# Optimization experiments

Measured on AMD Instinct MI355X. Metric: run time of the kernel, lower is better.

## Reference

```python
import jax, jax.numpy as jnp
import numpy as np

H, I, E, S, K = 768, 3072, 16, 2, 2
SCALE = 1.0  # routed_scaling_factor


def setup_inputs() -> dict:
    key = jax.random.key(0)
    ks = jax.random.split(key, 8)
    sd = 0.02
    return {
        "hidden_states": jax.random.normal(ks[0], (2, 1024, H), jnp.float32),
        "gate_w": jax.random.normal(ks[1], (E, H), jnp.float32) * sd,   # router nn.Linear(H,E).weight
        "shared_wg": jax.random.normal(ks[2], (S, H, I), jnp.float32) * sd,
        "shared_wu": jax.random.normal(ks[3], (S, H, I), jnp.float32) * sd,
        "shared_wd": jax.random.normal(ks[4], (S, I, H), jnp.float32) * sd,
        "wg": jax.random.normal(ks[5], (E, H, I), jnp.float32) * sd,
        "wu": jax.random.normal(ks[6], (E, H, I), jnp.float32) * sd,
        "wd": jax.random.normal(ks[7], (E, I, H), jnp.float32) * sd,
    }


def reference(hidden_states, gate_w, shared_wg, shared_wu, shared_wd, wg, wu, wd):
    B, T, _ = hidden_states.shape
    x = hidden_states.reshape(-1, H)                       # [N, H], N = B*T
    N = x.shape[0]

    # ---- shared experts: always-on, averaged ----
    g = jnp.einsum('nh,shi->sni', x, shared_wg)
    u = jnp.einsum('nh,shi->sni', x, shared_wu)
    shared_out = jnp.einsum('sni,sih->snh', jax.nn.silu(g) * u, shared_wd).mean(axis=0)

    # ---- router: softmax scores, top-k, renormalize, scale ----
    router_logits = x @ gate_w.T                           # [N, E]
    routing_weights = jax.nn.softmax(router_logits, axis=-1)
    topk_w, topk_idx = jax.lax.top_k(routing_weights, K)   # [N, K]
    topk_w = topk_w / (topk_w.sum(axis=-1, keepdims=True) + 1e-8)
    topk_w = topk_w * SCALE

    # combine weights: [N, E], zero for non-selected experts (duplicates summed,
    # matching the torch per-token weight-sum semantics)
    combine = jnp.zeros((N, E), x.dtype).at[jnp.arange(N)[:, None], topk_idx].add(topk_w)

    # ---- routed experts: weighted combine (w=0 for unselected -> same math) ----
    ge = jnp.einsum('nh,ehi->eni', x, wg)                  # [E, N, I]
    ue = jnp.einsum('nh,ehi->eni', x, wu)
    ye = jnp.einsum('eni,eih->enh', jax.nn.silu(ge) * ue, wd)  # [E, N, H]
    routed_out = jnp.einsum('ne,enh->nh', combine, ye)

    return (shared_out + routed_out).reshape(B, T, H)
```

## Files before the change

### kernel.cpp

```cpp
#include <hip/hip_runtime.h>
#include <hip/hip_bf16.h>

#define H 768
#define I_DIM 3072
#define NEXP 16
#define TOPK 2

typedef __bf16 bf16;
typedef __bf16 bf16x4 __attribute__((ext_vector_type(4)));
typedef __bf16 bf16x8 __attribute__((ext_vector_type(8)));
typedef float f32x4 __attribute__((ext_vector_type(4)));

__device__ __forceinline__ int swizzle_mtile(int bx, int gx) {
    int per = gx >> 3;
    if ((per << 3) != gx) return bx;
    return (bx & 7) * per + (bx >> 3);
}

__global__ void cvt_x_kernel(const float* __restrict__ x, bf16* __restrict__ xb, int n) {
    int i = (blockIdx.x * blockDim.x + threadIdx.x) * 8;
    if (i >= n) return;
    f32x4 v0 = *(const f32x4*)(x + i);
    f32x4 v1 = *(const f32x4*)(x + i + 4);
    bf16x8 p;
#pragma unroll
    for (int j = 0; j < 4; j++) { p[j] = (bf16)v0[j]; p[4 + j] = (bf16)v1[j]; }
    *(bf16x8*)(xb + i) = p;
}

__global__ __launch_bounds__(256) void transpose_cvt_kernel(
        const float* __restrict__ in, bf16* __restrict__ outp, int R, int C) {
    __shared__ bf16 t[64][74];
    const float* ip = in + (size_t)blockIdx.z * R * C;
    bf16* op = outp + (size_t)blockIdx.z * R * C;
    int c0 = blockIdx.x * 64, r0 = blockIdx.y * 64;
    int tid = threadIdx.x;
    int lr = tid >> 4, lc = (tid & 15) * 4;
#pragma unroll
    for (int p = 0; p < 4; p++) {
        int r = p * 16 + lr;
        f32x4 v = *(const f32x4*)(ip + (size_t)(r0 + r) * C + (c0 + lc));
        bf16x4 b;
#pragma unroll
        for (int j = 0; j < 4; j++) b[j] = (bf16)v[j];
        *(bf16x4*)&t[r][lc] = b;
    }
    __syncthreads();
    int oc = tid >> 2, s = (tid & 3) * 16;
    bf16x8 o0, o1;
#pragma unroll
    for (int j = 0; j < 8; j++) { o0[j] = t[s + j][oc]; o1[j] = t[s + 8 + j][oc]; }
    *(bf16x8*)(op + (size_t)(c0 + oc) * R + (r0 + s)) = o0;
    *(bf16x8*)(op + (size_t)(c0 + oc) * R + (r0 + s + 8)) = o1;
}

__global__ void router_kernel(const float* __restrict__ x, const float* __restrict__ gw,
                              int* __restrict__ tk_e, float* __restrict__ tk_w,
                              int* __restrict__ counts, int N) {
    int wave = threadIdx.x >> 6;
    int lane = threadIdx.x & 63;
    int t = blockIdx.x * 4 + wave;
    if (t >= N) return;
    const float* xr = x + (size_t)t * H;
    float acc[NEXP];
#pragma unroll
    for (int e = 0; e < NEXP; e++) acc[e] = 0.f;
    for (int h0 = 0; h0 < H; h0 += 64) {
        float xv = xr[h0 + lane];
#pragma unroll
        for (int e = 0; e < NEXP; e++) acc[e] += xv * gw[e * H + h0 + lane];
    }
#pragma unroll
    for (int e = 0; e < NEXP; e++) {
#pragma unroll
        for (int off = 32; off > 0; off >>= 1) acc[e] += __shfl_xor(acc[e], off);
    }
    if (lane == 0) {
        float m = acc[0];
#pragma unroll
        for (int e = 1; e < NEXP; e++) m = fmaxf(m, acc[e]);
        float p[NEXP]; float z = 0.f;
#pragma unroll
        for (int e = 0; e < NEXP; e++) { p[e] = expf(acc[e] - m); z += p[e]; }
        float inv = 1.f / z;
#pragma unroll
        for (int e = 0; e < NEXP; e++) p[e] *= inv;
        int i0 = 0; float v0 = p[0];
#pragma unroll
        for (int e = 1; e < NEXP; e++) if (p[e] > v0) { v0 = p[e]; i0 = e; }
        int i1 = -1; float v1 = -1.f;
#pragma unroll
        for (int e = 0; e < NEXP; e++) if (e != i0 && p[e] > v1) { v1 = p[e]; i1 = e; }
        float s = 1.f / (v0 + v1 + 1e-8f);
        tk_e[t * 2 + 0] = i0; tk_w[t * 2 + 0] = v0 * s;
        tk_e[t * 2 + 1] = i1; tk_w[t * 2 + 1] = v1 * s;
        atomicAdd(&counts[i0], 1);
        atomicAdd(&counts[i1], 1);
    }
}

__global__ void scan_fill_kernel(const int* __restrict__ counts, int* __restrict__ cursors,
                                 int* __restrict__ pad_off, int* __restrict__ rows_token,
                                 float* __restrict__ rows_weight, int N) {
    __shared__ int s_total;
    if (threadIdx.x == 0) {
        int off = 0;
        for (int e = 0; e < NEXP; e++) {
            pad_off[e] = off;
            cursors[e] = off;
            off += (counts[e] + 127) & ~127;
        }
        pad_off[NEXP] = off;
        s_total = off;
    }
    __syncthreads();
    int total = s_total;
    for (int r = threadIdx.x; r < 2 * N; r += blockDim.x) {
        rows_token[r] = r & (N - 1);
        rows_weight[r] = 0.5f;
    }
    for (int r = threadIdx.x; r < total; r += blockDim.x) {
        rows_token[2 * N + r] = 0;
        rows_weight[2 * N + r] = 0.f;
    }
}

__global__ void scatter_kernel(const int* __restrict__ tk_e, const float* __restrict__ tk_w,
                               int* __restrict__ cursors, int* __restrict__ rows_token,
                               float* __restrict__ rows_weight, int N) {
    int i = blockIdx.x * blockDim.x + threadIdx.x;
    if (i >= N * TOPK) return;
    int e = tk_e[i];
    int pos = atomicAdd(&cursors[e], 1);
    rows_token[2 * N + pos] = i >> 1;
    rows_weight[2 * N + pos] = tk_w[i];
}

__global__ __launch_bounds__(256) void phaseA_t_kernel(
        const bf16* __restrict__ xb, const bf16* __restrict__ WgT, const bf16* __restrict__ WuT,
        const int* __restrict__ pad_off, const int* __restrict__ rows_token,
        bf16* __restrict__ P, int N, int ic0, int ichunk) {
    int mtile = swizzle_mtile(blockIdx.x, gridDim.x);
    int ntile = blockIdx.y;
    int sh_tiles = (2 * N) / 128;
    int rowbase; const bf16* gptr; const bf16* uptr;
    if (mtile < sh_tiles) {
        rowbase = mtile * 128;
        int s = rowbase / N;
        gptr = WgT + (size_t)s * I_DIM * H;
        uptr = WuT + (size_t)s * I_DIM * H;
    } else {
        int rm = (mtile - sh_tiles) * 128;
        if (rm >= pad_off[NEXP]) return;
        int e = NEXP - 1;
        for (int q = 0; q < NEXP; q++) { if (rm < pad_off[q + 1]) { e = q; break; } }
        rowbase = 2 * N + rm;
        gptr = WgT + (size_t)(2 + e) * I_DIM * H;
        uptr = WuT + (size_t)(2 + e) * I_DIM * H;
    }
    int icol0 = ic0 + ntile * 64;
    int pcol0 = ntile * 64;

    __shared__ bf16 As[2][128][40];
    __shared__ bf16 Bgs[2][64][40];
    __shared__ bf16 Bus[2][64][40];
    __shared__ int sTok[128];

    int tid = threadIdx.x;
    if (tid < 128) sTok[tid] = rows_token[rowbase + tid];
    __syncthreads();

    f32x4 accG[4][2], accU[4][2];
#pragma unroll
    for (int i = 0; i < 4; i++)
#pragma unroll
        for (int j = 0; j < 2; j++) {
            accG[i][j] = (f32x4){0.f, 0.f, 0.f, 0.f};
            accU[i][j] = (f32x4){0.f, 0.f, 0.f, 0.f};
        }

    int ar = tid >> 1, ah = tid & 1;
    const bf16* arow = xb + (size_t)sTok[ar] * H + ah * 16;
    int bn = tid >> 2, bkq = tid & 3;
    const bf16* gb = gptr + (size_t)(icol0 + bn) * H + bkq * 8;
    const bf16* ub = uptr + (size_t)(icol0 + bn) * H + bkq * 8;

    int lane = tid & 63, w = tid >> 6;
    int wm = (w & 1) * 64, wn = (w >> 1) * 32;
    int fr = lane & 15, fq = (lane >> 4) * 8;

    bf16x8 rA0, rA1, rG, rU;

#define PAT_LOADK(kk)                                                         \
    {                                                                         \
        rA0 = *(const bf16x8*)(arow + (kk));                                  \
        rA1 = *(const bf16x8*)(arow + (kk) + 8);                              \
        rG = *(const bf16x8*)(gb + (kk));                                     \
        rU = *(const bf16x8*)(ub + (kk));                                     \
    }
#define PAT_STORE(buf)                                                        \
    {                                                                         \
        *(bf16x8*)&As[buf][ar][ah * 16] = rA0;                                \
        *(bf16x8*)&As[buf][ar][ah * 16 + 8] = rA1;                            \
        *(bf16x8*)&Bgs[buf][bn][bkq * 8] = rG;                                \
        *(bf16x8*)&Bus[buf][bn][bkq * 8] = rU;                                \
    }

    PAT_LOADK(0);
    PAT_STORE(0);
    __syncthreads();

#pragma unroll
    for (int kb = 0; kb < 24; kb++) {
        if (kb < 23) PAT_LOADK((kb + 1) * 32);
        int cur = kb & 1;
        bf16x8 a[4], bg[2], bu[2];
#pragma unroll
        for (int mi = 0; mi < 4; mi++) a[mi] = *(const bf16x8*)&As[cur][wm + mi * 16 + fr][fq];
#pragma unroll
        for (int ni = 0; ni < 2; ni++) {
            bg[ni] = *(const bf16x8*)&Bgs[cur][wn + ni * 16 + fr][fq];
            bu[ni] = *(const bf16x8*)&Bus[cur][wn + ni * 16 + fr][fq];
        }
#pragma unroll
        for (int mi = 0; mi < 4; mi++)
#pragma unroll
            for (int ni = 0; ni < 2; ni++) {
                accG[mi][ni] = __builtin_amdgcn_mfma_f32_16x16x32_bf16(a[mi], bg[ni], accG[mi][ni], 0, 0, 0);
                accU[mi][ni] = __builtin_amdgcn_mfma_f32_16x16x32_bf16(a[mi], bu[ni], accU[mi][ni], 0, 0, 0);
            }
        if (kb < 23) {
            PAT_STORE(cur ^ 1);
            __syncthreads();
        }
    }

    int cq = lane >> 4;
#pragma unroll
    for (int mi = 0; mi < 4; mi++)
#pragma unroll
        for (int ni = 0; ni < 2; ni++) {
            int n = wn + ni * 16 + fr;
#pragma unroll
            for (int rr = 0; rr < 4; rr++) {
                int m = wm + mi * 16 + cq * 4 + rr;
                float g = accG[mi][ni][rr];
                float u = accU[mi][ni][rr];
                float pv = (g / (1.f + __expf(-g))) * u;
                P[(size_t)(rowbase + m) * ichunk + pcol0 + n] = (bf16)pv;
            }
        }
}

__global__ __launch_bounds__(256) void phaseB_t_kernel(
        const bf16* __restrict__ P, const bf16* __restrict__ WdT,
        const int* __restrict__ pad_off, const int* __restrict__ rows_token,
        const float* __restrict__ rows_weight, float* __restrict__ out,
        int N, int ic0, int ichunk) {
    int mtile = swizzle_mtile(blockIdx.x, gridDim.x);
    int ntile = blockIdx.y;
    int sh_tiles = (2 * N) / 128;
    int rowbase; const bf16* dptr;
    if (mtile < sh_tiles) {
        rowbase = mtile * 128;
        int s = rowbase / N;
        dptr = WdT + (size_t)s * I_DIM * H;
    } else {
        int rm = (mtile - sh_tiles) * 128;
        if (rm >= pad_off[NEXP]) return;
        int e = NEXP - 1;
        for (int q = 0; q < NEXP; q++) { if (rm < pad_off[q + 1]) { e = q; break; } }
        rowbase = 2 * N + rm;
        dptr = WdT + (size_t)(2 + e) * I_DIM * H;
    }
    int h0 = ntile * 128;

    __shared__ bf16 As[2][128][40];
    __shared__ bf16 Bs[2][128][40];
    __shared__ int sTok[128];
    __shared__ float sW[128];

    int tid = threadIdx.x;
    if (tid < 128) {
        sTok[tid] = rows_token[rowbase + tid];
        sW[tid] = rows_weight[rowbase + tid];
    }
    __syncthreads();

    f32x4 acc[4][4];
#pragma unroll
    for (int i = 0; i < 4; i++)
#pragma unroll
        for (int j = 0; j < 4; j++) acc[i][j] = (f32x4){0.f, 0.f, 0.f, 0.f};

    int ar = tid >> 1, ah = tid & 1;
    const bf16* arow = P + (size_t)(rowbase + ar) * ichunk + ah * 16;
    int bn = tid >> 1, bkh = tid & 1;
    const bf16* db = dptr + (size_t)(h0 + bn) * I_DIM + ic0 + bkh * 16;

    int lane = tid & 63, w = tid >> 6;
    int wm = (w & 1) * 64, wn = (w >> 1) * 64;
    int fr = lane & 15, fq = (lane >> 4) * 8;

    bf16x8 rA0, rA1, rB0, rB1;

#define PBT_LOADK(kk)                                                         \
    {                                                                         \
        rA0 = *(const bf16x8*)(arow + (kk));                                  \
        rA1 = *(const bf16x8*)(arow + (kk) + 8);                              \
        rB0 = *(const bf16x8*)(db + (kk));                                    \
        rB1 = *(const bf16x8*)(db + (kk) + 8);                                \
    }
#define PBT_STORE(buf)                                                        \
    {                                                                         \
        *(bf16x8*)&As[buf][ar][ah * 16] = rA0;                                \
        *(bf16x8*)&As[buf][ar][ah * 16 + 8] = rA1;                            \
        *(bf16x8*)&Bs[buf][bn][bkh * 16] = rB0;                               \
        *(bf16x8*)&Bs[buf][bn][bkh * 16 + 8] = rB1;                           \
    }

    PBT_LOADK(0);
    PBT_STORE(0);
    __syncthreads();

    int KB = ichunk >> 5;
    for (int kb = 0; kb < KB; kb++) {
        if (kb + 1 < KB) PBT_LOADK((kb + 1) * 32);
        int cur = kb & 1;
        bf16x8 a[4], b[4];
#pragma unroll
        for (int mi = 0; mi < 4; mi++) a[mi] = *(const bf16x8*)&As[cur][wm + mi * 16 + fr][fq];
#pragma unroll
        for (int ni = 0; ni < 4; ni++) b[ni] = *(const bf16x8*)&Bs[cur][wn + ni * 16 + fr][fq];
#pragma unroll
        for (int mi = 0; mi < 4; mi++)
#pragma unroll
            for (int ni = 0; ni < 4; ni++)
                acc[mi][ni] = __builtin_amdgcn_mfma_f32_16x16x32_bf16(a[mi], b[ni], acc[mi][ni], 0, 0, 0);
        if (kb + 1 < KB) {
            PBT_STORE(cur ^ 1);
            __syncthreads();
        }
    }

    int cq = lane >> 4;
#pragma unroll
    for (int mi = 0; mi < 4; mi++)
#pragma unroll
        for (int ni = 0; ni < 4; ni++) {
            int n = wn + ni * 16 + fr;
#pragma unroll
            for (int rr = 0; rr < 4; rr++) {
                int m = wm + mi * 16 + cq * 4 + rr;
                atomicAdd(&out[(size_t)sTok[m] * H + h0 + n], sW[m] * acc[mi][ni][rr]);
            }
        }
}

__global__ __launch_bounds__(256) void phaseA_kernel(
        const bf16* __restrict__ xb, const float* __restrict__ swg, const float* __restrict__ swu,
        const float* __restrict__ wg, const float* __restrict__ wu,
        const int* __restrict__ pad_off, const int* __restrict__ rows_token,
        bf16* __restrict__ P, int N, int ic0, int ichunk) {
    int mtile = swizzle_mtile(blockIdx.x, gridDim.x);
    int ntile = blockIdx.y;
    int sh_tiles = (2 * N) / 128;
    int rowbase; const float* gptr; const float* uptr;
    if (mtile < sh_tiles) {
        rowbase = mtile * 128;
        int s = rowbase / N;
        gptr = swg + (size_t)s * H * I_DIM;
        uptr = swu + (size_t)s * H * I_DIM;
    } else {
        int rm = (mtile - sh_tiles) * 128;
        if (rm >= pad_off[NEXP]) return;
        int e = NEXP - 1;
        for (int q = 0; q < NEXP; q++) { if (rm < pad_off[q + 1]) { e = q; break; } }
        rowbase = 2 * N + rm;
        gptr = wg + (size_t)e * H * I_DIM;
        uptr = wu + (size_t)e * H * I_DIM;
    }
    int icol0 = ic0 + ntile * 64;
    int pcol0 = ntile * 64;

    __shared__ bf16 As[2][128][40];
    __shared__ bf16 Bgs[2][64][40];
    __shared__ bf16 Bus[2][64][40];
    __shared__ int sTok[128];

    int tid = threadIdx.x;
    if (tid < 128) sTok[tid] = rows_token[rowbase + tid];
    __syncthreads();

    f32x4 accG[4][2], accU[4][2];
#pragma unroll
    for (int i = 0; i < 4; i++)
#pragma unroll
        for (int j = 0; j < 2; j++) {
            accG[i][j] = (f32x4){0.f, 0.f, 0.f, 0.f};
            accU[i][j] = (f32x4){0.f, 0.f, 0.f, 0.f};
        }

    int ar = tid >> 1, ah = tid & 1;
    const bf16* arow = xb + (size_t)sTok[ar] * H + ah * 16;
    int bn = tid & 63, bkq = tid >> 6;
    const float* gbase = gptr + icol0 + bn;
    const float* ubase = uptr + icol0 + bn;

    int lane = tid & 63, w = tid >> 6;
    int wm = (w & 1) * 64, wn = (w >> 1) * 32;
    int fr = lane & 15, fq = (lane >> 4) * 8;

    bf16x8 rA0, rA1;
    float gv[8], uv[8];

#define PA_LOADK(kk)                                                          \
    {                                                                         \
        rA0 = *(const bf16x8*)(arow + (kk));                                  \
        rA1 = *(const bf16x8*)(arow + (kk) + 8);                              \
        _Pragma("unroll")                                                     \
        for (int j = 0; j < 8; j++) {                                         \
            gv[j] = gbase[(size_t)((kk) + bkq * 8 + j) * I_DIM];              \
            uv[j] = ubase[(size_t)((kk) + bkq * 8 + j) * I_DIM];              \
        }                                                                     \
    }
#define PA_STORE(buf)                                                         \
    {                                                                         \
        *(bf16x8*)&As[buf][ar][ah * 16] = rA0;                                \
        *(bf16x8*)&As[buf][ar][ah * 16 + 8] = rA1;                            \
        bf16x8 pg, pu;                                                        \
        _Pragma("unroll")                                                     \
        for (int j = 0; j < 8; j++) { pg[j] = (bf16)gv[j]; pu[j] = (bf16)uv[j]; } \
        *(bf16x8*)&Bgs[buf][bn][bkq * 8] = pg;                                \
        *(bf16x8*)&Bus[buf][bn][bkq * 8] = pu;                                \
    }

    PA_LOADK(0);
    PA_STORE(0);
    __syncthreads();

#pragma unroll
    for (int kb = 0; kb < 24; kb++) {
        if (kb < 23) PA_LOADK((kb + 1) * 32);
        int cur = kb & 1;
        bf16x8 a[4], bg[2], bu[2];
#pragma unroll
        for (int mi = 0; mi < 4; mi++) a[mi] = *(const bf16x8*)&As[cur][wm + mi * 16 + fr][fq];
#pragma unroll
        for (int ni = 0; ni < 2; ni++) {
            bg[ni] = *(const bf16x8*)&Bgs[cur][wn + ni * 16 + fr][fq];
            bu[ni] = *(const bf16x8*)&Bus[cur][wn + ni * 16 + fr][fq];
        }
#pragma unroll
        for (int mi = 0; mi < 4; mi++)
#pragma unroll
            for (int ni = 0; ni < 2; ni++) {
                accG[mi][ni] = __builtin_amdgcn_mfma_f32_16x16x32_bf16(a[mi], bg[ni], accG[mi][ni], 0, 0, 0);
                accU[mi][ni] = __builtin_amdgcn_mfma_f32_16x16x32_bf16(a[mi], bu[ni], accU[mi][ni], 0, 0, 0);
            }
        if (kb < 23) {
            PA_STORE(cur ^ 1);
            __syncthreads();
        }
    }

    int cq = lane >> 4;
#pragma unroll
    for (int mi = 0; mi < 4; mi++)
#pragma unroll
        for (int ni = 0; ni < 2; ni++) {
            int n = wn + ni * 16 + fr;
#pragma unroll
            for (int rr = 0; rr < 4; rr++) {
                int m = wm + mi * 16 + cq * 4 + rr;
                float g = accG[mi][ni][rr];
                float u = accU[mi][ni][rr];
                float pv = (g / (1.f + __expf(-g))) * u;
                P[(size_t)(rowbase + m) * ichunk + pcol0 + n] = (bf16)pv;
            }
        }
}

__global__ __launch_bounds__(256) void phaseB_kernel(
        const bf16* __restrict__ P, const float* __restrict__ swd, const float* __restrict__ wd,
        const int* __restrict__ pad_off, const int* __restrict__ rows_token,
        const float* __restrict__ rows_weight, float* __restrict__ out,
        int N, int ic0, int ichunk) {
    int mtile = swizzle_mtile(blockIdx.x, gridDim.x);
    int ntile = blockIdx.y;
    int sh_tiles = (2 * N) / 128;
    int rowbase; const float* dptr;
    if (mtile < sh_tiles) {
        rowbase = mtile * 128;
        int s = rowbase / N;
        dptr = swd + (size_t)s * I_DIM * H;
    } else {
        int rm = (mtile - sh_tiles) * 128;
        if (rm >= pad_off[NEXP]) return;
        int e = NEXP - 1;
        for (int q = 0; q < NEXP; q++) { if (rm < pad_off[q + 1]) { e = q; break; } }
        rowbase = 2 * N + rm;
        dptr = wd + (size_t)e * I_DIM * H;
    }
    int h0 = ntile * 128;

    __shared__ bf16 As[2][128][40];
    __shared__ bf16 Bs[2][128][40];
    __shared__ int sTok[128];
    __shared__ float sW[128];

    int tid = threadIdx.x;
    if (tid < 128) {
        sTok[tid] = rows_token[rowbase + tid];
        sW[tid] = rows_weight[rowbase + tid];
    }
    __syncthreads();

    f32x4 acc[4][4];
#pragma unroll
    for (int i = 0; i < 4; i++)
#pragma unroll
        for (int j = 0; j < 4; j++) acc[i][j] = (f32x4){0.f, 0.f, 0.f, 0.f};

    int ar = tid >> 1, ah = tid & 1;
    const bf16* arow = P + (size_t)(rowbase + ar) * ichunk + ah * 16;
    int bcol = tid & 127, bko = (tid >> 7) * 16;
    const float* dbase = dptr + (size_t)ic0 * H + h0 + bcol;

    int lane = tid & 63, w = tid >> 6;
    int wm = (w & 1) * 64, wn = (w >> 1) * 64;
    int fr = lane & 15, fq = (lane >> 4) * 8;

    bf16x8 rA0, rA1;
    float dv[16];

#define PB_LOADK(kk)                                                          \
    {                                                                         \
        rA0 = *(const bf16x8*)(arow + (kk));                                  \
        rA1 = *(const bf16x8*)(arow + (kk) + 8);                              \
        _Pragma("unroll")                                                     \
        for (int j = 0; j < 16; j++)                                          \
            dv[j] = dbase[(size_t)((kk) + bko + j) * H];                      \
    }
#define PB_STORE(buf)                                                         \
    {                                                                         \
        *(bf16x8*)&As[buf][ar][ah * 16] = rA0;                                \
        *(bf16x8*)&As[buf][ar][ah * 16 + 8] = rA1;                            \
        bf16x8 p0, p1;                                                        \
        _Pragma("unroll")                                                     \
        for (int j = 0; j < 8; j++) { p0[j] = (bf16)dv[j]; p1[j] = (bf16)dv[8 + j]; } \
        *(bf16x8*)&Bs[buf][bcol][bko] = p0;                                   \
        *(bf16x8*)&Bs[buf][bcol][bko + 8] = p1;                               \
    }

    PB_LOADK(0);
    PB_STORE(0);
    __syncthreads();

    int KB = ichunk >> 5;
    for (int kb = 0; kb < KB; kb++) {
        if (kb + 1 < KB) PB_LOADK((kb + 1) * 32);
        int cur = kb & 1;
        bf16x8 a[4], b[4];
#pragma unroll
        for (int mi = 0; mi < 4; mi++) a[mi] = *(const bf16x8*)&As[cur][wm + mi * 16 + fr][fq];
#pragma unroll
        for (int ni = 0; ni < 4; ni++) b[ni] = *(const bf16x8*)&Bs[cur][wn + ni * 16 + fr][fq];
#pragma unroll
        for (int mi = 0; mi < 4; mi++)
#pragma unroll
            for (int ni = 0; ni < 4; ni++)
                acc[mi][ni] = __builtin_amdgcn_mfma_f32_16x16x32_bf16(a[mi], b[ni], acc[mi][ni], 0, 0, 0);
        if (kb + 1 < KB) {
            PB_STORE(cur ^ 1);
            __syncthreads();
        }
    }

    int cq = lane >> 4;
#pragma unroll
    for (int mi = 0; mi < 4; mi++)
#pragma unroll
        for (int ni = 0; ni < 4; ni++) {
            int n = wn + ni * 16 + fr;
#pragma unroll
            for (int rr = 0; rr < 4; rr++) {
                int m = wm + mi * 16 + cq * 4 + rr;
                atomicAdd(&out[(size_t)sTok[m] * H + h0 + n], sW[m] * acc[mi][ni][rr]);
            }
        }
}

extern "C" void kernel_launch(void* const* d_in, const int* in_sizes, int n_in,
                              void* d_out, int out_size, void* d_ws, size_t ws_size,
                              hipStream_t stream) {
    const float* x   = (const float*)d_in[0];
    const float* gw  = (const float*)d_in[1];
    const float* swg = (const float*)d_in[2];
    const float* swu = (const float*)d_in[3];
    const float* swd = (const float*)d_in[4];
    const float* wg  = (const float*)d_in[5];
    const float* wu  = (const float*)d_in[6];
    const float* wd  = (const float*)d_in[7];
    float* out = (float*)d_out;

    int N = in_sizes[0] / H;
    int ROWCAP = 2 * N + N * TOPK + NEXP * 128;

    int* wsi = (int*)d_ws;
    int* counts     = wsi + 0;
    int* cursors    = wsi + 16;
    int* pad_off    = wsi + 32;
    int* tk_e       = wsi + 64;
    float* tk_w     = (float*)(wsi + 64 + 2 * N);
    int* rows_token = wsi + 64 + 4 * N;
    float* rows_weight = (float*)(wsi + 64 + 4 * N + ROWCAP);

    size_t xb_off = 131072;
    bf16* xb = (bf16*)((char*)d_ws + xb_off);
    size_t pbase = xb_off + (size_t)N * H * 2;

    const int cand[10] = {3072, 1536, 1024, 768, 512, 384, 256, 192, 128, 64};

    size_t MATEL = (size_t)I_DIM * H;
    size_t WB = 18 * MATEL * 2;
    size_t wt_off = pbase;
    size_t p2base = wt_off + 3 * WB;
    int ichunk2 = 0;
    for (int i = 0; i < 10; i++) {
        if (p2base + (size_t)ROWCAP * cand[i] * 2 <= ws_size) { ichunk2 = cand[i]; break; }
    }

    hipMemsetAsync(d_out, 0, (size_t)out_size * sizeof(float), stream);
    hipMemsetAsync(d_ws, 0, 256, stream);

    cvt_x_kernel<<<(N * H) / 2048, 256, 0, stream>>>(x, xb, N * H);
    router_kernel<<<(N + 3) / 4, 256, 0, stream>>>(x, gw, tk_e, tk_w, counts, N);
    scan_fill_kernel<<<1, 256, 0, stream>>>(counts, cursors, pad_off, rows_token, rows_weight, N);
    scatter_kernel<<<(N * TOPK + 255) / 256, 256, 0, stream>>>(tk_e, tk_w, cursors, rows_token, rows_weight, N);

    int sh_tiles = (2 * N) / 128;
    int rt_tiles = (N * TOPK + NEXP * 128) / 128;

    if (ichunk2 > 0) {
        bf16* WgT = (bf16*)((char*)d_ws + wt_off);
        bf16* WuT = WgT + 18 * MATEL;
        bf16* WdT = WuT + 18 * MATEL;
        bf16* P = (bf16*)((char*)d_ws + p2base);
        int ichunk = ichunk2;

        transpose_cvt_kernel<<<dim3(I_DIM / 64, H / 64, 2), 256, 0, stream>>>(swg, WgT, H, I_DIM);
        transpose_cvt_kernel<<<dim3(I_DIM / 64, H / 64, 16), 256, 0, stream>>>(wg, WgT + 2 * MATEL, H, I_DIM);
        transpose_cvt_kernel<<<dim3(I_DIM / 64, H / 64, 2), 256, 0, stream>>>(swu, WuT, H, I_DIM);
        transpose_cvt_kernel<<<dim3(I_DIM / 64, H / 64, 16), 256, 0, stream>>>(wu, WuT + 2 * MATEL, H, I_DIM);
        transpose_cvt_kernel<<<dim3(H / 64, I_DIM / 64, 2), 256, 0, stream>>>(swd, WdT, I_DIM, H);
        transpose_cvt_kernel<<<dim3(H / 64, I_DIM / 64, 16), 256, 0, stream>>>(wd, WdT + 2 * MATEL, I_DIM, H);

        for (int ic0 = 0; ic0 < I_DIM; ic0 += ichunk) {
            dim3 gA(sh_tiles + rt_tiles, ichunk / 64);
            phaseA_t_kernel<<<gA, dim3(256), 0, stream>>>(xb, WgT, WuT, pad_off, rows_token, P, N, ic0, ichunk);
            dim3 gB(sh_tiles + rt_tiles, H / 128);
            phaseB_t_kernel<<<gB, dim3(256), 0, stream>>>(P, WdT, pad_off, rows_token, rows_weight, out, N, ic0, ichunk);
        }
    } else {
        int ichunk = 64;
        for (int i = 0; i < 10; i++) {
            if (pbase + (size_t)ROWCAP * cand[i] * 2 <= ws_size) { ichunk = cand[i]; break; }
        }
        bf16* P = (bf16*)((char*)d_ws + pbase);
        for (int ic0 = 0; ic0 < I_DIM; ic0 += ichunk) {
            dim3 gA(sh_tiles + rt_tiles, ichunk / 64);
            phaseA_kernel<<<gA, dim3(256), 0, stream>>>(xb, swg, swu, wg, wu, pad_off, rows_token, P, N, ic0, ichunk);
            dim3 gB(sh_tiles + rt_tiles, H / 128);
            phaseB_kernel<<<gB, dim3(256), 0, stream>>>(P, swd, wd, pad_off, rows_token, rows_weight, out, N, ic0, ichunk);
        }
    }
}
```

Before: 880.8 us.

## Split-K the down-projection GEMM and merge weight transpose launches

```diff
diff --git a/kernel.cpp b/kernel.cpp
--- a/kernel.cpp
+++ b/kernel.cpp
@@ -10,6 +10,8 @@
 typedef __bf16 bf16x4 __attribute__((ext_vector_type(4)));
 typedef __bf16 bf16x8 __attribute__((ext_vector_type(8)));
 typedef float f32x4 __attribute__((ext_vector_type(4)));
+
+#define MATEL ((size_t)I_DIM * H)
 
 __device__ __forceinline__ int swizzle_mtile(int bx, int gx) {
     int per = gx >> 3;
@@ -28,11 +30,9 @@
     *(bf16x8*)(xb + i) = p;
 }
 
-__global__ __launch_bounds__(256) void transpose_cvt_kernel(
-        const float* __restrict__ in, bf16* __restrict__ outp, int R, int C) {
+__device__ __forceinline__ void transpose_tile(const float* __restrict__ ip,
+                                               bf16* __restrict__ op, int R, int C) {
     __shared__ bf16 t[64][74];
-    const float* ip = in + (size_t)blockIdx.z * R * C;
-    bf16* op = outp + (size_t)blockIdx.z * R * C;
     int c0 = blockIdx.x * 64, r0 = blockIdx.y * 64;
     int tid = threadIdx.x;
     int lr = tid >> 4, lc = (tid & 15) * 4;
@@ -52,6 +52,28 @@
     for (int j = 0; j < 8; j++) { o0[j] = t[s + j][oc]; o1[j] = t[s + 8 + j][oc]; }
     *(bf16x8*)(op + (size_t)(c0 + oc) * R + (r0 + s)) = o0;
     *(bf16x8*)(op + (size_t)(c0 + oc) * R + (r0 + s + 8)) = o1;
+}
+
+__global__ __launch_bounds__(256) void transpose_gu_kernel(
+        const float* __restrict__ swg, const float* __restrict__ wg,
+        const float* __restrict__ swu, const float* __restrict__ wu,
+        bf16* __restrict__ WgT, bf16* __restrict__ WuT) {
+    int z = blockIdx.z;
+    const float* src; bf16* dst;
+    if (z < 2)       { src = swg + (size_t)z * MATEL;        dst = WgT + (size_t)z * MATEL; }
+    else if (z < 18) { src = wg  + (size_t)(z - 2) * MATEL;  dst = WgT + (size_t)z * MATEL; }
+    else if (z < 20) { src = swu + (size_t)(z - 18) * MATEL; dst = WuT + (size_t)(z - 18) * MATEL; }
+    else             { src = wu  + (size_t)(z - 20) * MATEL; dst = WuT + (size_t)(z - 18) * MATEL; }
+    transpose_tile(src, dst, H, I_DIM);
+}
+
+__global__ __launch_bounds__(256) void transpose_d_kernel(
+        const float* __restrict__ swd, const float* __restrict__ wd, bf16* __restrict__ WdT) {
+    int z = blockIdx.z;
+    const float* src; bf16* dst;
+    if (z < 2) { src = swd + (size_t)z * MATEL;       dst = WdT + (size_t)z * MATEL; }
+    else       { src = wd  + (size_t)(z - 2) * MATEL; dst = WdT + (size_t)z * MATEL; }
+    transpose_tile(src, dst, I_DIM, H);
 }
 
 __global__ void router_kernel(const float* __restrict__ x, const float* __restrict__ gw,
@@ -147,16 +169,16 @@
     if (mtile < sh_tiles) {
         rowbase = mtile * 128;
         int s = rowbase / N;
-        gptr = WgT + (size_t)s * I_DIM * H;
-        uptr = WuT + (size_t)s * I_DIM * H;
+        gptr = WgT + (size_t)s * MATEL;
+        uptr = WuT + (size_t)s * MATEL;
     } else {
         int rm = (mtile - sh_tiles) * 128;
         if (rm >= pad_off[NEXP]) return;
         int e = NEXP - 1;
         for (int q = 0; q < NEXP; q++) { if (rm < pad_off[q + 1]) { e = q; break; } }
         rowbase = 2 * N + rm;
-        gptr = WgT + (size_t)(2 + e) * I_DIM * H;
-        uptr = WuT + (size_t)(2 + e) * I_DIM * H;
+        gptr = WgT + (size_t)(2 + e) * MATEL;
+        uptr = WuT + (size_t)(2 + e) * MATEL;
     }
     int icol0 = ic0 + ntile * 64;
     int pcol0 = ntile * 64;
@@ -256,22 +278,23 @@
         const bf16* __restrict__ P, const bf16* __restrict__ WdT,
         const int* __restrict__ pad_off, const int* __restrict__ rows_token,
         const float* __restrict__ rows_weight, float* __restrict__ out,
-        int N, int ic0, int ichunk) {
+        int N, int ic0, int ichunk, int KSEG) {
     int mtile = swizzle_mtile(blockIdx.x, gridDim.x);
     int ntile = blockIdx.y;
+    int kseg0 = blockIdx.z * KSEG;
     int sh_tiles = (2 * N) / 128;
     int rowbase; const bf16* dptr;
     if (mtile < sh_tiles) {
         rowbase = mtile * 128;
         int s = rowbase / N;
-        dptr = WdT + (size_t)s * I_DIM * H;
+        dptr = WdT + (size_t)s * MATEL;
     } else {
         int rm = (mtile - sh_tiles) * 128;
         if (rm >= pad_off[NEXP]) return;
         int e = NEXP - 1;
         for (int q = 0; q < NEXP; q++) { if (rm < pad_off[q + 1]) { e = q; break; } }
         rowbase = 2 * N + rm;
-        dptr = WdT + (size_t)(2 + e) * I_DIM * H;
+        dptr = WdT + (size_t)(2 + e) * MATEL;
     }
     int h0 = ntile * 128;
 
@@ -294,9 +317,9 @@
         for (int j = 0; j < 4; j++) acc[i][j] = (f32x4){0.f, 0.f, 0.f, 0.f};
 
     int ar = tid >> 1, ah = tid & 1;
-    const bf16* arow = P + (size_t)(rowbase + ar) * ichunk + ah * 16;
+    const bf16* arow = P + (size_t)(rowbase + ar) * ichunk + kseg0 + ah * 16;
     int bn = tid >> 1, bkh = tid & 1;
-    const bf16* db = dptr + (size_t)(h0 + bn) * I_DIM + ic0 + bkh * 16;
+    const bf16* db = dptr + (size_t)(h0 + bn) * I_DIM + ic0 + kseg0 + bkh * 16;
 
     int lane = tid & 63, w = tid >> 6;
     int wm = (w & 1) * 64, wn = (w >> 1) * 64;
@@ -323,7 +346,7 @@
     PBT_STORE(0);
     __syncthreads();
 
-    int KB = ichunk >> 5;
+    int KB = KSEG >> 5;
     for (int kb = 0; kb < KB; kb++) {
         if (kb + 1 < KB) PBT_LOADK((kb + 1) * 32);
         int cur = kb & 1;
@@ -622,7 +645,6 @@
 
     const int cand[10] = {3072, 1536, 1024, 768, 512, 384, 256, 192, 128, 64};
 
-    size_t MATEL = (size_t)I_DIM * H;
     size_t WB = 18 * MATEL * 2;
     size_t wt_off = pbase;
     size_t p2base = wt_off + 3 * WB;
@@ -649,18 +671,20 @@
         bf16* P = (bf16*)((char*)d_ws + p2base);
         int ichunk = ichunk2;
 
-        transpose_cvt_kernel<<<dim3(I_DIM / 64, H / 64, 2), 256, 0, stream>>>(swg, WgT, H, I_DIM);
-        transpose_cvt_kernel<<<dim3(I_DIM / 64, H / 64, 16), 256, 0, stream>>>(wg, WgT + 2 * MATEL, H, I_DIM);
-        transpose_cvt_kernel<<<dim3(I_DIM / 64, H / 64, 2), 256, 0, stream>>>(swu, WuT, H, I_DIM);
-        transpose_cvt_kernel<<<dim3(I_DIM / 64, H / 64, 16), 256, 0, stream>>>(wu, WuT + 2 * MATEL, H, I_DIM);
-        transpose_cvt_kernel<<<dim3(H / 64, I_DIM / 64, 2), 256, 0, stream>>>(swd, WdT, I_DIM, H);
-        transpose_cvt_kernel<<<dim3(H / 64, I_DIM / 64, 16), 256, 0, stream>>>(wd, WdT + 2 * MATEL, I_DIM, H);
+        transpose_gu_kernel<<<dim3(I_DIM / 64, H / 64, 36), 256, 0, stream>>>(swg, wg, swu, wu, WgT, WuT);
+        transpose_d_kernel<<<dim3(H / 64, I_DIM / 64, 18), 256, 0, stream>>>(swd, wd, WdT);
+
+        int KSEG = ichunk;
+        const int segc[4] = {768, 512, 384, 256};
+        for (int i = 0; i < 4; i++) {
+            if (ichunk > segc[i] && ichunk % segc[i] == 0) { KSEG = segc[i]; break; }
+        }
 
         for (int ic0 = 0; ic0 < I_DIM; ic0 += ichunk) {
             dim3 gA(sh_tiles + rt_tiles, ichunk / 64);
             phaseA_t_kernel<<<gA, dim3(256), 0, stream>>>(xb, WgT, WuT, pad_off, rows_token, P, N, ic0, ichunk);
-            dim3 gB(sh_tiles + rt_tiles, H / 128);
-            phaseB_t_kernel<<<gB, dim3(256), 0, stream>>>(P, WdT, pad_off, rows_token, rows_weight, out, N, ic0, ichunk);
+            dim3 gB(sh_tiles + rt_tiles, H / 128, ichunk / KSEG);
+            phaseB_t_kernel<<<gB, dim3(256), 0, stream>>>(P, WdT, pad_off, rows_token, rows_weight, out, N, ic0, ichunk, KSEG);
         }
     } else {
         int ichunk = 64;
```

Measured after the change: 1.193 ms. 35.4% more time.
